# Performance work log

Measured on AMD Instinct MI355X. Metric: run time of the kernel, lower is better.

## Reference

```python
import jax, jax.numpy as jnp
import numpy as np

N_NODES = 50000
N_EDGES = 600000
DIM = 128
N_HEADS = 3
EDGE_VOCAB = 22754
NEG_SLOPE = 0.2


def setup_inputs() -> dict:
    key = jax.random.key(0)
    ks = jax.random.split(key, 12)
    s = 1.0 / np.sqrt(DIM)
    return {
        "x": jax.random.normal(ks[0], (N_NODES, DIM), dtype=jnp.float32),
        "edge_index": jax.random.randint(ks[1], (2, N_EDGES), 0, N_NODES, dtype=jnp.int64),
        "edge_ids": jax.random.randint(ks[2], (N_EDGES,), 0, EDGE_VOCAB, dtype=jnp.int64),
        "ddi_weight": jax.random.uniform(ks[3], (N_EDGES,), dtype=jnp.float32),
        "W_lin": jax.random.normal(ks[4], (DIM, DIM), dtype=jnp.float32) * s,
        "b_lin": jnp.zeros((DIM,), dtype=jnp.float32),
        "edge_emb": jax.random.normal(ks[5], (EDGE_VOCAB, 1), dtype=jnp.float32) * 0.1,
        "W_heads": jax.random.normal(ks[6], (N_HEADS, DIM, DIM), dtype=jnp.float32) * s,
        "att_src": jax.random.normal(ks[7], (N_HEADS, DIM), dtype=jnp.float32) * s,
        "att_dst": jax.random.normal(ks[8], (N_HEADS, DIM), dtype=jnp.float32) * s,
        "bias_heads": jnp.zeros((N_HEADS, DIM), dtype=jnp.float32),
    }


def _gat_head(x, src, dst, ew, W, a_src, a_dst, bias):
    # x: [N, D] (already passed through shared lin), ew: [E] scalar edge weights
    h = x @ W                                   # [N, D]
    e = jax.nn.leaky_relu(
        (h @ a_src)[src] + (h @ a_dst)[dst], NEG_SLOPE)   # [E]
    # segment softmax over destination nodes
    e_max = jax.ops.segment_max(e, dst, num_segments=N_NODES)   # [N]
    e_exp = jnp.exp(e - e_max[dst])                              # [E]
    denom = jax.ops.segment_sum(e_exp, dst, num_segments=N_NODES)
    alpha = e_exp / jnp.maximum(denom[dst], 1e-16)               # [E]
    msg = (alpha * ew)[:, None] * h[src]                         # [E, D]
    return jax.ops.segment_sum(msg, dst, num_segments=N_NODES) + bias


def reference(x, edge_index, edge_ids, ddi_weight, W_lin, b_lin, edge_emb,
              W_heads, att_src, att_dst, bias_heads):
    x = x @ W_lin + b_lin                         # shared linear projection
    ew = edge_emb[edge_ids, 0] - ddi_weight        # [E]
    src, dst = edge_index[0], edge_index[1]
    out = jnp.zeros_like(x)
    for hix in range(N_HEADS):                     # small fixed head count
        out = out + _gat_head(x, src, dst, ew, W_heads[hix],
                              att_src[hix], att_dst[hix], bias_heads[hix])
    return out / N_HEADS
```

## Files before the change

kernel.cpp:

```cpp
#include <hip/hip_runtime.h>
#include <math.h>

#define NN 50000
#define NE 600000
#define D 128
#define NH 3
#define CAP 64
#define ZERO_BLOCKS ((NN + 255) / 256)

typedef short bf16x8 __attribute__((ext_vector_type(8)));
typedef float f32x4 __attribute__((ext_vector_type(4)));

__device__ __forceinline__ unsigned short f2b(float f) {
  unsigned int u = __float_as_uint(f);
  u += 0x7FFF + ((u >> 16) & 1);
  return (unsigned short)(u >> 16);
}
__device__ __forceinline__ float blo(unsigned int u) {
  return __uint_as_float(u << 16);
}
__device__ __forceinline__ float bhi(unsigned int u) {
  return __uint_as_float(u & 0xffff0000u);
}

__global__ __launch_bounds__(256) void pack_all(const float* __restrict__ W_lin,
                                                const float* __restrict__ W_heads,
                                                const float* __restrict__ att_src,
                                                const float* __restrict__ att_dst,
                                                const float* __restrict__ b_lin,
                                                uint4* __restrict__ Bpack,
                                                float* __restrict__ bcomb,
                                                float* __restrict__ sbuf,
                                                int* __restrict__ counts) {
  const int bx = blockIdx.x;
  const int tid = threadIdx.x;
  if (bx < 24) {
    int u = bx * 256 + tid;
    int h = u >> 11, r = u & 2047;
    int nt = r >> 8, s = (r >> 6) & 3, q = (r >> 4) & 3, n0 = r & 15;
    int kbase = s * 32 + q * 8;
    int n = nt * 16 + n0;
    const float* wl = W_lin + kbase * D;
    const float* wh = W_heads + h * D * D + n;
    float vals[8];
    #pragma unroll
    for (int j = 0; j < 8; ++j) vals[j] = 0.f;
    for (int m = 0; m < D; ++m) {
      float whv = wh[m * D];
      #pragma unroll
      for (int j = 0; j < 8; ++j) vals[j] += wl[j * D + m] * whv;
    }
    unsigned int w[4];
    #pragma unroll
    for (int p = 0; p < 4; ++p)
      w[p] = (unsigned int)f2b(vals[2 * p]) | ((unsigned int)f2b(vals[2 * p + 1]) << 16);
    Bpack[h * 2304 + r] = make_uint4(w[0], w[1], w[2], w[3]);
  } else if (bx < 27) {
    const int h = bx - 24;
    __shared__ float wha_s[128], wha_d[128], scs[128], scd[128];
    {
      int m = tid & 127;
      const float* W = W_heads + h * D * D + m * D;
      const float* a = (tid < 128) ? (att_src + h * D) : (att_dst + h * D);
      float acc = 0.f;
      for (int n = 0; n < D; ++n) acc += W[n] * a[n];
      if (tid < 128) wha_s[m] = acc; else wha_d[m] = acc;
    }
    __syncthreads();
    {
      int k = tid & 127;
      const float* wl = W_lin + k * D;
      const float* wha = (tid < 128) ? wha_s : wha_d;
      float acc = 0.f;
      for (int m = 0; m < D; ++m) acc += wl[m] * wha[m];
      if (tid < 128) scs[k] = acc; else scd[k] = acc;
    }
    __syncthreads();
    if (tid < 2) {
      const float* wha = tid ? wha_d : wha_s;
      float a = 0.f;
      for (int k = 0; k < D; ++k) a += b_lin[k] * wha[k];
      sbuf[h * 2 + tid] = a;
    }
    {
      int s = (tid >> 6) & 3, q = (tid >> 4) & 3, n0 = tid & 15;
      int kbase = s * 32 + q * 8;
      float vals[8];
      #pragma unroll
      for (int j = 0; j < 8; ++j)
        vals[j] = (n0 == 0) ? scs[kbase + j] : ((n0 == 1) ? scd[kbase + j] : 0.f);
      unsigned int w[4];
      #pragma unroll
      for (int p = 0; p < 4; ++p)
        w[p] = (unsigned int)f2b(vals[2 * p]) | ((unsigned int)f2b(vals[2 * p + 1]) << 16);
      Bpack[h * 2304 + 2048 + tid] = make_uint4(w[0], w[1], w[2], w[3]);
    }
  } else if (bx < 29) {
    int t = (bx - 27) * 256 + tid;
    if (t < NH * D) {
      int h = t / D, n = t - h * D;
      float acc = 0.f;
      for (int k = 0; k < D; ++k) acc += b_lin[k] * W_heads[h * D * D + k * D + n];
      bcomb[t] = acc;
    }
  } else {
    int i = (bx - 29) * 256 + tid;
    if (i < NN) counts[i] = 0;
  }
}

__global__ __launch_bounds__(256) void mfma_h3s(const float* __restrict__ x,
                                                const uint4* __restrict__ Bpack,
                                                const float* __restrict__ bcomb,
                                                const float* __restrict__ sbuf,
                                                unsigned short* __restrict__ h3,
                                                float* __restrict__ s_src4,
                                                float* __restrict__ s_dst4) {
  const int head = blockIdx.y;
  const int row0 = blockIdx.x * 64;
  const int tid = threadIdx.x;
  __shared__ __align__(16) unsigned short As[64][136];
  #pragma unroll
  for (int it = 0; it < 8; ++it) {
    int idx = tid + it * 256;
    int m = idx >> 5, k4 = idx & 31;
    int row = row0 + m;
    float4 v = make_float4(0.f, 0.f, 0.f, 0.f);
    if (row < NN) v = ((const float4*)(x + (size_t)row * D))[k4];
    uint2 pk;
    pk.x = (unsigned int)f2b(v.x) | ((unsigned int)f2b(v.y) << 16);
    pk.y = (unsigned int)f2b(v.z) | ((unsigned int)f2b(v.w) << 16);
    *((uint2*)&As[m][k4 * 4]) = pk;
  }
  __syncthreads();
  const int wv = tid >> 6;
  const int lane = tid & 63;
  const int n0 = lane & 15, q = lane >> 4;
  const int boff = q * 16 + n0;
  const bf16x8* Bp = (const bf16x8*)(Bpack + head * 2304);

  bf16x8 a4[4];
  #pragma unroll
  for (int s = 0; s < 4; ++s)
    a4[s] = *(const bf16x8*)&As[wv * 16 + n0][s * 32 + q * 8];

  f32x4 acc[9];
  #pragma unroll
  for (int nt = 0; nt < 9; ++nt) acc[nt] = (f32x4){0.f, 0.f, 0.f, 0.f};

  #pragma unroll
  for (int s = 0; s < 4; ++s) {
    #pragma unroll
    for (int nt = 0; nt < 9; ++nt) {
      bf16x8 b = Bp[(nt * 4 + s) * 64 + boff];
      acc[nt] = __builtin_amdgcn_mfma_f32_16x16x32_bf16(a4[s], b, acc[nt], 0, 0, 0);
    }
  }
  __syncthreads();
  const float* bc = bcomb + head * D;
  #pragma unroll
  for (int nt = 0; nt < 8; ++nt) {
    int col = nt * 16 + n0;
    float bv = bc[col];
    #pragma unroll
    for (int r = 0; r < 4; ++r)
      As[wv * 16 + q * 4 + r][col] = f2b(acc[nt][r] + bv);
  }
  if (n0 < 2) {
    float sb = sbuf[head * 2 + n0];
    float* Sout = n0 ? s_dst4 : s_src4;
    #pragma unroll
    for (int r = 0; r < 4; ++r) {
      int row = row0 + wv * 16 + q * 4 + r;
      if (row < NN) Sout[row * 4 + head] = acc[8][r] + sb;
    }
  }
  __syncthreads();
  #pragma unroll
  for (int i = 0; i < 4; ++i) {
    int idx = tid + i * 256;
    int row = idx >> 4, c16 = idx & 15;
    int grow = row0 + row;
    if (grow < NN)
      *((uint4*)&h3[(size_t)grow * (NH * D) + head * D + c16 * 8]) =
          *((const uint4*)&As[row][c16 * 8]);
  }
}

__global__ __launch_bounds__(256) void scatter(const int* __restrict__ ei,
                                               const int* __restrict__ eid,
                                               const float* __restrict__ ddi,
                                               const float* __restrict__ emb,
                                               const float4* __restrict__ s_src4,
                                               const float4* __restrict__ s_dst4,
                                               int* __restrict__ counts,
                                               float4* __restrict__ slots) {
  int e = blockIdx.x * 256 + threadIdx.x;
  if (e >= NE) return;
  int src = ei[e], dst = ei[NE + e];
  int idx = atomicAdd(&counts[dst], 1);
  idx = idx < CAP ? idx : CAP - 1;
  float ew = emb[eid[e]] - ddi[e];
  float4 ss = s_src4[src];
  float4 sd = s_dst4[dst];
  float v0 = ss.x + sd.x, v1 = ss.y + sd.y, v2 = ss.z + sd.z;
  v0 = v0 > 0.f ? v0 : 0.2f * v0;
  v1 = v1 > 0.f ? v1 : 0.2f * v1;
  v2 = v2 > 0.f ? v2 : 0.2f * v2;
  float p0 = __expf(v0), p1 = __expf(v1), p2 = __expf(v2);
  unsigned int se = (unsigned int)src | ((unsigned int)f2b(ew) << 16);
  slots[dst * CAP + idx] = make_float4(__uint_as_float(se), p0, p1, p2);
}

__global__ __launch_bounds__(64) void gather9(const int* __restrict__ counts,
                                              const float4* __restrict__ slots,
                                              const unsigned short* __restrict__ h3,
                                              const float* __restrict__ bias_heads,
                                              float* __restrict__ out) {
  const int dst = blockIdx.x;
  const int lane = threadIdx.x;
  const int half = lane >> 5;
  const int c = (lane & 31) * 4;
  int cnt = counts[dst];
  cnt = cnt < CAP ? cnt : CAP;
  const int beg = dst * CAP;
  const int end = beg + cnt;
  float a0[4] = {0.f, 0.f, 0.f, 0.f};
  float a1[4] = {0.f, 0.f, 0.f, 0.f};
  float a2[4] = {0.f, 0.f, 0.f, 0.f};
  float d0 = 0.f, d1 = 0.f, d2 = 0.f;
  int s = beg + half;
  for (; s + 2 < end; s += 4) {
    float4 A = slots[s];
    float4 B = slots[s + 2];
    unsigned int seA = __float_as_uint(A.x);
    unsigned int seB = __float_as_uint(B.x);
    const unsigned short* ha = h3 + (size_t)(seA & 0xffffu) * (NH * D);
    const unsigned short* hb = h3 + (size_t)(seB & 0xffffu) * (NH * D);
    float ewA = bhi(seA), ewB = bhi(seB);
    uint2 ua0 = *(const uint2*)&ha[c];
    uint2 ua1 = *(const uint2*)&ha[D + c];
    uint2 ua2 = *(const uint2*)&ha[2 * D + c];
    uint2 ub0 = *(const uint2*)&hb[c];
    uint2 ub1 = *(const uint2*)&hb[D + c];
    uint2 ub2 = *(const uint2*)&hb[2 * D + c];
    float wa0 = A.y * ewA, wa1 = A.z * ewA, wa2 = A.w * ewA;
    float wb0 = B.y * ewB, wb1 = B.z * ewB, wb2 = B.w * ewB;
    a0[0] += wa0 * blo(ua0.x) + wb0 * blo(ub0.x);
    a0[1] += wa0 * bhi(ua0.x) + wb0 * bhi(ub0.x);
    a0[2] += wa0 * blo(ua0.y) + wb0 * blo(ub0.y);
    a0[3] += wa0 * bhi(ua0.y) + wb0 * bhi(ub0.y);
    a1[0] += wa1 * blo(ua1.x) + wb1 * blo(ub1.x);
    a1[1] += wa1 * bhi(ua1.x) + wb1 * bhi(ub1.x);
    a1[2] += wa1 * blo(ua1.y) + wb1 * blo(ub1.y);
    a1[3] += wa1 * bhi(ua1.y) + wb1 * bhi(ub1.y);
    a2[0] += wa2 * blo(ua2.x) + wb2 * blo(ub2.x);
    a2[1] += wa2 * bhi(ua2.x) + wb2 * bhi(ub2.x);
    a2[2] += wa2 * blo(ua2.y) + wb2 * blo(ub2.y);
    a2[3] += wa2 * bhi(ua2.y) + wb2 * bhi(ub2.y);
    d0 += A.y + B.y;
    d1 += A.z + B.z;
    d2 += A.w + B.w;
  }
  if (s < end) {
    float4 A = slots[s];
    unsigned int seA = __float_as_uint(A.x);
    const unsigned short* hp = h3 + (size_t)(seA & 0xffffu) * (NH * D);
    float ew = bhi(seA);
    uint2 u0 = *(const uint2*)&hp[c];
    uint2 u1 = *(const uint2*)&hp[D + c];
    uint2 u2 = *(const uint2*)&hp[2 * D + c];
    float w0 = A.y * ew, w1 = A.z * ew, w2 = A.w * ew;
    a0[0] += w0 * blo(u0.x); a0[1] += w0 * bhi(u0.x);
    a0[2] += w0 * blo(u0.y); a0[3] += w0 * bhi(u0.y);
    a1[0] += w1 * blo(u1.x); a1[1] += w1 * bhi(u1.x);
    a1[2] += w1 * blo(u1.y); a1[3] += w1 * bhi(u1.y);
    a2[0] += w2 * blo(u2.x); a2[1] += w2 * bhi(u2.x);
    a2[2] += w2 * blo(u2.y); a2[3] += w2 * bhi(u2.y);
    d0 += A.y; d1 += A.z; d2 += A.w;
  }
  #pragma unroll
  for (int j = 0; j < 4; ++j) {
    a0[j] += __shfl_xor(a0[j], 32, 64);
    a1[j] += __shfl_xor(a1[j], 32, 64);
    a2[j] += __shfl_xor(a2[j], 32, 64);
  }
  d0 += __shfl_xor(d0, 32, 64);
  d1 += __shfl_xor(d1, 32, 64);
  d2 += __shfl_xor(d2, 32, 64);
  if (half == 0) {
    float r0 = 1.f / fmaxf(d0, 1e-16f);
    float r1 = 1.f / fmaxf(d1, 1e-16f);
    float r2 = 1.f / fmaxf(d2, 1e-16f);
    float4 b0 = ((const float4*)bias_heads)[lane & 31];
    float4 b1 = ((const float4*)bias_heads)[32 + (lane & 31)];
    float4 b2 = ((const float4*)bias_heads)[64 + (lane & 31)];
    float4 o;
    o.x = (a0[0] * r0 + a1[0] * r1 + a2[0] * r2 + b0.x + b1.x + b2.x) * (1.f / 3.f);
    o.y = (a0[1] * r0 + a1[1] * r1 + a2[1] * r2 + b0.y + b1.y + b2.y) * (1.f / 3.f);
    o.z = (a0[2] * r0 + a1[2] * r1 + a2[2] * r2 + b0.z + b1.z + b2.z) * (1.f / 3.f);
    o.w = (a0[3] * r0 + a1[3] * r1 + a2[3] * r2 + b0.w + b1.w + b2.w) * (1.f / 3.f);
    *((float4*)&out[(size_t)dst * D + c]) = o;
  }
}

extern "C" void kernel_launch(void* const* d_in, const int* in_sizes, int n_in,
                              void* d_out, int out_size, void* d_ws, size_t ws_size,
                              hipStream_t stream) {
  const float* x          = (const float*)d_in[0];
  const int*   ei         = (const int*)d_in[1];
  const int*   eid        = (const int*)d_in[2];
  const float* ddi        = (const float*)d_in[3];
  const float* W_lin      = (const float*)d_in[4];
  const float* b_lin      = (const float*)d_in[5];
  const float* emb        = (const float*)d_in[6];
  const float* W_heads    = (const float*)d_in[7];
  const float* att_src    = (const float*)d_in[8];
  const float* att_dst    = (const float*)d_in[9];
  const float* bias_heads = (const float*)d_in[10];
  float* out = (float*)d_out;

  float4* slots  = (float4*)d_ws;
  uint4*  Bpack  = (uint4*)(slots + (size_t)NN * CAP);
  unsigned short* h3 = (unsigned short*)(Bpack + NH * 2304);
  float*  bcomb  = (float*)(h3 + (size_t)NN * NH * D);
  float*  sbuf   = bcomb + NH * D;
  float*  s_src4 = sbuf + 8;
  float*  s_dst4 = s_src4 + (size_t)NN * 4;
  int*    counts = (int*)(s_dst4 + (size_t)NN * 4);

  const int edgeBlocks = (NE + 255) / 256;

  pack_all<<<29 + ZERO_BLOCKS, 256, 0, stream>>>(W_lin, W_heads, att_src, att_dst,
                                                 b_lin, Bpack, bcomb, sbuf, counts);
  mfma_h3s<<<dim3((NN + 63) / 64, NH), 256, 0, stream>>>(x, Bpack, bcomb, sbuf,
                                                         h3, s_src4, s_dst4);
  scatter<<<edgeBlocks, 256, 0, stream>>>(ei, eid, ddi, emb,
                                          (const float4*)s_src4, (const float4*)s_dst4,
                                          counts, slots);
  gather9<<<NN, 64, 0, stream>>>(counts, slots, h3, bias_heads, out);
}
```

Before: 238.3 us.

## Fuse edge bucketing into pack kernel and compute attention exps in gather

Result: faster. 229.6 us (-3.7%).

```diff
diff --git a/kernel.cpp b/kernel.cpp
--- a/kernel.cpp
+++ b/kernel.cpp
@@ -6,7 +6,7 @@
 #define D 128
 #define NH 3
 #define CAP 64
-#define ZERO_BLOCKS ((NN + 255) / 256)
+#define EDGE_BLOCKS ((NE + 255) / 256)
 
 typedef short bf16x8 __attribute__((ext_vector_type(8)));
 typedef float f32x4 __attribute__((ext_vector_type(4)));
@@ -23,15 +23,20 @@
   return __uint_as_float(u & 0xffff0000u);
 }
 
-__global__ __launch_bounds__(256) void pack_all(const float* __restrict__ W_lin,
-                                                const float* __restrict__ W_heads,
-                                                const float* __restrict__ att_src,
-                                                const float* __restrict__ att_dst,
-                                                const float* __restrict__ b_lin,
-                                                uint4* __restrict__ Bpack,
-                                                float* __restrict__ bcomb,
-                                                float* __restrict__ sbuf,
-                                                int* __restrict__ counts) {
+__global__ __launch_bounds__(256) void pack_scatter(const float* __restrict__ W_lin,
+                                                    const float* __restrict__ W_heads,
+                                                    const float* __restrict__ att_src,
+                                                    const float* __restrict__ att_dst,
+                                                    const float* __restrict__ b_lin,
+                                                    const int* __restrict__ ei,
+                                                    const int* __restrict__ eid,
+                                                    const float* __restrict__ ddi,
+                                                    const float* __restrict__ emb,
+                                                    uint4* __restrict__ Bpack,
+                                                    float* __restrict__ bcomb,
+                                                    float* __restrict__ sbuf,
+                                                    int* __restrict__ counts,
+                                                    unsigned int* __restrict__ slots8) {
   const int bx = blockIdx.x;
   const int tid = threadIdx.x;
   if (bx < 24) {
@@ -104,8 +109,14 @@
       bcomb[t] = acc;
     }
   } else {
-    int i = (bx - 29) * 256 + tid;
-    if (i < NN) counts[i] = 0;
+    int e = (bx - 29) * 256 + tid;
+    if (e < NE) {
+      int src = ei[e], dst = ei[NE + e];
+      int idx = atomicAdd(&counts[dst], 1);
+      idx = idx < CAP ? idx : CAP - 1;
+      float ew = emb[eid[e]] - ddi[e];
+      slots8[dst * CAP + idx] = (unsigned int)src | ((unsigned int)f2b(ew) << 16);
+    }
   }
 }
 
@@ -187,36 +198,13 @@
   }
 }
 
-__global__ __launch_bounds__(256) void scatter(const int* __restrict__ ei,
-                                               const int* __restrict__ eid,
-                                               const float* __restrict__ ddi,
-                                               const float* __restrict__ emb,
+__global__ __launch_bounds__(64) void gather10(const int* __restrict__ counts,
+                                               const unsigned int* __restrict__ slots8,
                                                const float4* __restrict__ s_src4,
                                                const float4* __restrict__ s_dst4,
-                                               int* __restrict__ counts,
-                                               float4* __restrict__ slots) {
-  int e = blockIdx.x * 256 + threadIdx.x;
-  if (e >= NE) return;
-  int src = ei[e], dst = ei[NE + e];
-  int idx = atomicAdd(&counts[dst], 1);
-  idx = idx < CAP ? idx : CAP - 1;
-  float ew = emb[eid[e]] - ddi[e];
-  float4 ss = s_src4[src];
-  float4 sd = s_dst4[dst];
-  float v0 = ss.x + sd.x, v1 = ss.y + sd.y, v2 = ss.z + sd.z;
-  v0 = v0 > 0.f ? v0 : 0.2f * v0;
-  v1 = v1 > 0.f ? v1 : 0.2f * v1;
-  v2 = v2 > 0.f ? v2 : 0.2f * v2;
-  float p0 = __expf(v0), p1 = __expf(v1), p2 = __expf(v2);
-  unsigned int se = (unsigned int)src | ((unsigned int)f2b(ew) << 16);
-  slots[dst * CAP + idx] = make_float4(__uint_as_float(se), p0, p1, p2);
-}
-
-__global__ __launch_bounds__(64) void gather9(const int* __restrict__ counts,
-                                              const float4* __restrict__ slots,
-                                              const unsigned short* __restrict__ h3,
-                                              const float* __restrict__ bias_heads,
-                                              float* __restrict__ out) {
+                                               const unsigned short* __restrict__ h3,
+                                               const float* __restrict__ bias_heads,
+                                               float* __restrict__ out) {
   const int dst = blockIdx.x;
   const int lane = threadIdx.x;
   const int half = lane >> 5;
@@ -225,27 +213,39 @@
   cnt = cnt < CAP ? cnt : CAP;
   const int beg = dst * CAP;
   const int end = beg + cnt;
+  float4 sd = s_dst4[dst];
   float a0[4] = {0.f, 0.f, 0.f, 0.f};
   float a1[4] = {0.f, 0.f, 0.f, 0.f};
   float a2[4] = {0.f, 0.f, 0.f, 0.f};
   float d0 = 0.f, d1 = 0.f, d2 = 0.f;
   int s = beg + half;
   for (; s + 2 < end; s += 4) {
-    float4 A = slots[s];
-    float4 B = slots[s + 2];
-    unsigned int seA = __float_as_uint(A.x);
-    unsigned int seB = __float_as_uint(B.x);
-    const unsigned short* ha = h3 + (size_t)(seA & 0xffffu) * (NH * D);
-    const unsigned short* hb = h3 + (size_t)(seB & 0xffffu) * (NH * D);
+    unsigned int seA = slots8[s];
+    unsigned int seB = slots8[s + 2];
+    int srcA = seA & 0xffffu, srcB = seB & 0xffffu;
     float ewA = bhi(seA), ewB = bhi(seB);
+    float4 ssA = s_src4[srcA];
+    float4 ssB = s_src4[srcB];
+    const unsigned short* ha = h3 + (size_t)srcA * (NH * D);
+    const unsigned short* hb = h3 + (size_t)srcB * (NH * D);
     uint2 ua0 = *(const uint2*)&ha[c];
     uint2 ua1 = *(const uint2*)&ha[D + c];
     uint2 ua2 = *(const uint2*)&ha[2 * D + c];
     uint2 ub0 = *(const uint2*)&hb[c];
     uint2 ub1 = *(const uint2*)&hb[D + c];
     uint2 ub2 = *(const uint2*)&hb[2 * D + c];
-    float wa0 = A.y * ewA, wa1 = A.z * ewA, wa2 = A.w * ewA;
-    float wb0 = B.y * ewB, wb1 = B.z * ewB, wb2 = B.w * ewB;
+    float vA0 = ssA.x + sd.x, vA1 = ssA.y + sd.y, vA2 = ssA.z + sd.z;
+    float vB0 = ssB.x + sd.x, vB1 = ssB.y + sd.y, vB2 = ssB.z + sd.z;
+    vA0 = vA0 > 0.f ? vA0 : 0.2f * vA0;
+    vA1 = vA1 > 0.f ? vA1 : 0.2f * vA1;
+    vA2 = vA2 > 0.f ? vA2 : 0.2f * vA2;
+    vB0 = vB0 > 0.f ? vB0 : 0.2f * vB0;
+    vB1 = vB1 > 0.f ? vB1 : 0.2f * vB1;
+    vB2 = vB2 > 0.f ? vB2 : 0.2f * vB2;
+    float pA0 = __expf(vA0), pA1 = __expf(vA1), pA2 = __expf(vA2);
+    float pB0 = __expf(vB0), pB1 = __expf(vB1), pB2 = __expf(vB2);
+    float wa0 = pA0 * ewA, wa1 = pA1 * ewA, wa2 = pA2 * ewA;
+    float wb0 = pB0 * ewB, wb1 = pB1 * ewB, wb2 = pB2 * ewB;
     a0[0] += wa0 * blo(ua0.x) + wb0 * blo(ub0.x);
     a0[1] += wa0 * bhi(ua0.x) + wb0 * bhi(ub0.x);
     a0[2] += wa0 * blo(ua0.y) + wb0 * blo(ub0.y);
@@ -258,26 +258,32 @@
     a2[1] += wa2 * bhi(ua2.x) + wb2 * bhi(ub2.x);
     a2[2] += wa2 * blo(ua2.y) + wb2 * blo(ub2.y);
     a2[3] += wa2 * bhi(ua2.y) + wb2 * bhi(ub2.y);
-    d0 += A.y + B.y;
-    d1 += A.z + B.z;
-    d2 += A.w + B.w;
+    d0 += pA0 + pB0;
+    d1 += pA1 + pB1;
+    d2 += pA2 + pB2;
   }
   if (s < end) {
-    float4 A = slots[s];
-    unsigned int seA = __float_as_uint(A.x);
-    const unsigned short* hp = h3 + (size_t)(seA & 0xffffu) * (NH * D);
-    float ew = bhi(seA);
+    unsigned int seA = slots8[s];
+    int srcA = seA & 0xffffu;
+    float ewA = bhi(seA);
+    float4 ssA = s_src4[srcA];
+    const unsigned short* hp = h3 + (size_t)srcA * (NH * D);
     uint2 u0 = *(const uint2*)&hp[c];
     uint2 u1 = *(const uint2*)&hp[D + c];
     uint2 u2 = *(const uint2*)&hp[2 * D + c];
-    float w0 = A.y * ew, w1 = A.z * ew, w2 = A.w * ew;
+    float vA0 = ssA.x + sd.x, vA1 = ssA.y + sd.y, vA2 = ssA.z + sd.z;
+    vA0 = vA0 > 0.f ? vA0 : 0.2f * vA0;
+    vA1 = vA1 > 0.f ? vA1 : 0.2f * vA1;
+    vA2 = vA2 > 0.f ? vA2 : 0.2f * vA2;
+    float pA0 = __expf(vA0), pA1 = __expf(vA1), pA2 = __expf(vA2);
+    float w0 = pA0 * ewA, w1 = pA1 * ewA, w2 = pA2 * ewA;
     a0[0] += w0 * blo(u0.x); a0[1] += w0 * bhi(u0.x);
     a0[2] += w0 * blo(u0.y); a0[3] += w0 * bhi(u0.y);
     a1[0] += w1 * blo(u1.x); a1[1] += w1 * bhi(u1.x);
     a1[2] += w1 * blo(u1.y); a1[3] += w1 * bhi(u1.y);
     a2[0] += w2 * blo(u2.x); a2[1] += w2 * bhi(u2.x);
     a2[2] += w2 * blo(u2.y); a2[3] += w2 * bhi(u2.y);
-    d0 += A.y; d1 += A.z; d2 += A.w;
+    d0 += pA0; d1 += pA1; d2 += pA2;
   }
   #pragma unroll
   for (int j = 0; j < 4; ++j) {
@@ -320,23 +326,22 @@
   const float* bias_heads = (const float*)d_in[10];
   float* out = (float*)d_out;
 
-  float4* slots  = (float4*)d_ws;
-  uint4*  Bpack  = (uint4*)(slots + (size_t)NN * CAP);
+  uint4*  Bpack  = (uint4*)d_ws;
   unsigned short* h3 = (unsigned short*)(Bpack + NH * 2304);
-  float*  bcomb  = (float*)(h3 + (size_t)NN * NH * D);
+  unsigned int* slots8 = (unsigned int*)(h3 + (size_t)NN * NH * D);
+  float*  bcomb  = (float*)(slots8 + (size_t)NN * CAP);
   float*  sbuf   = bcomb + NH * D;
   float*  s_src4 = sbuf + 8;
   float*  s_dst4 = s_src4 + (size_t)NN * 4;
   int*    counts = (int*)(s_dst4 + (size_t)NN * 4);
 
-  const int edgeBlocks = (NE + 255) / 256;
-
-  pack_all<<<29 + ZERO_BLOCKS, 256, 0, stream>>>(W_lin, W_heads, att_src, att_dst,
-                                                 b_lin, Bpack, bcomb, sbuf, counts);
+  hipMemsetAsync(counts, 0, (size_t)NN * sizeof(int), stream);
+  pack_scatter<<<29 + EDGE_BLOCKS, 256, 0, stream>>>(W_lin, W_heads, att_src,
+                                                     att_dst, b_lin, ei, eid, ddi,
+                                                     emb, Bpack, bcomb, sbuf,
+                                                     counts, slots8);
   mfma_h3s<<<dim3((NN + 63) / 64, NH), 256, 0, stream>>>(x, Bpack, bcomb, sbuf,
                                                          h3, s_src4, s_dst4);
-  scatter<<<edgeBlocks, 256, 0, stream>>>(ei, eid, ddi, emb,
-                                          (const float4*)s_src4, (const float4*)s_dst4,
-                                          counts, slots);
-  gather9<<<NN, 64, 0, stream>>>(counts, slots, h3, bias_heads, out);
-}
+  gather10<<<NN, 64, 0, stream>>>(counts, slots8, (const float4*)s_src4,
+                                  (const float4*)s_dst4, h3, bias_heads, out);
+}
```
